# Kernel optimization log

Hardware: AMD Instinct MI355X
Metric: run time of the kernel (lower is better)

## Reference

```python
import jax, jax.numpy as jnp
import numpy as np

B, S, H, F, E, TOPK = 2, 2048, 1024, 512, 8, 2


def setup_inputs() -> dict:
    key = jax.random.key(0)
    k1, k2, k3, k4, k5 = jax.random.split(key, 5)
    s_h = 1.0 / np.sqrt(H)
    s_f = 1.0 / np.sqrt(F)
    return {
        "x": jax.random.normal(k1, (B, S, H), dtype=jnp.float32),
        "Wr": jax.random.normal(k2, (H, E), dtype=jnp.float32) * s_h,   # router
        "Wg": jax.random.normal(k3, (E, H, F), dtype=jnp.float32) * s_h,  # gate proj
        "Wu": jax.random.normal(k4, (E, H, F), dtype=jnp.float32) * s_h,  # up proj
        "Wd": jax.random.normal(k5, (E, F, H), dtype=jnp.float32) * s_f,  # down proj
        "topk": TOPK,
    }


def reference(x, Wr, Wg, Wu, Wd, topk):
    Bq, Sq, Hq = x.shape
    Eq = Wr.shape[1]
    xf = x.reshape(-1, Hq)                      # [T, H]
    logits = xf @ Wr                            # [T, E]
    probs = jax.nn.softmax(logits, axis=-1)
    w, idx = jax.lax.top_k(probs, topk)         # [T, topk]
    w = w / jnp.sum(w, axis=-1, keepdims=True)  # normalize top-k probs (Qwen3-style)
    # combine coefficients per (token, expert): scatter top-k weights
    coeff = jnp.sum(jax.nn.one_hot(idx, Eq, dtype=w.dtype) * w[..., None], axis=1)  # [T, E]
    # dense dispatch/combine (math-equivalent to per-expert gather + scatter-add)
    gate = jnp.einsum('th,ehf->tef', xf, Wg)    # [T, E, F]
    up = jnp.einsum('th,ehf->tef', xf, Wu)
    act = jax.nn.silu(gate) * up                # SwiGLU expert
    # apply combine weight before down-proj (linearity) to avoid a [T,E,H] temp
    out = jnp.einsum('tef,efh->th', act * coeff[:, :, None], Wd)
    return out.reshape(Bq, Sq, Hq)
```

## Files before the change

kernel.cpp:

```cpp
#include <hip/hip_runtime.h>
#include <hip/hip_bf16.h>

#define T_TOK    4096
#define H_DIM    1024
#define F_DIM    512
#define N_EXP    8
#define N_ASSIGN 8192
#define BM 128
#define BN 128
#define BK 64
#define MAX_TILES 80
#define GRID_MT   71

typedef __bf16 bf16x8 __attribute__((ext_vector_type(8)));
typedef __bf16 bf16x2 __attribute__((ext_vector_type(2)));
typedef float  f32x4  __attribute__((ext_vector_type(4)));

#define MFMA16(a, b, c) __builtin_amdgcn_mfma_f32_16x16x32_bf16((a), (b), (c), 0, 0, 0)

__device__ __forceinline__ void gl_lds16(const __bf16* g, __bf16* l) {
    __builtin_amdgcn_global_load_lds(
        (const __attribute__((address_space(1))) unsigned int*)g,
        (__attribute__((address_space(3))) unsigned int*)l,
        16, 0, 0);
}

__global__ __launch_bounds__(256) void routing_kernel(
    const float* __restrict__ x, const float* __restrict__ Wr,
    __bf16* __restrict__ xb, int* __restrict__ top_e, float* __restrict__ top_w)
{
    int wave = threadIdx.x >> 6, lane = threadIdx.x & 63;
    int t = blockIdx.x * 4 + wave;
    const float* xrow = x + (size_t)t * H_DIM;
    __bf16* xbrow = xb + (size_t)t * H_DIM;

    float part[N_EXP];
#pragma unroll
    for (int e = 0; e < N_EXP; ++e) part[e] = 0.f;

#pragma unroll
    for (int half = 0; half < 2; ++half) {
        int h0 = half * 512 + lane * 8;
        float4 v0 = *(const float4*)(xrow + h0);
        float4 v1 = *(const float4*)(xrow + h0 + 4);
        float xs[8] = {v0.x, v0.y, v0.z, v0.w, v1.x, v1.y, v1.z, v1.w};
        bf16x8 bv;
#pragma unroll
        for (int i = 0; i < 8; ++i) bv[i] = (__bf16)xs[i];
        *(bf16x8*)(xbrow + h0) = bv;
#pragma unroll
        for (int i = 0; i < 8; ++i) {
            const float4* wr = (const float4*)(Wr + (size_t)(h0 + i) * N_EXP);
            float4 w0 = wr[0], w1 = wr[1];
            part[0] += xs[i] * w0.x; part[1] += xs[i] * w0.y;
            part[2] += xs[i] * w0.z; part[3] += xs[i] * w0.w;
            part[4] += xs[i] * w1.x; part[5] += xs[i] * w1.y;
            part[6] += xs[i] * w1.z; part[7] += xs[i] * w1.w;
        }
    }
#pragma unroll
    for (int m = 1; m < 64; m <<= 1) {
#pragma unroll
        for (int e = 0; e < N_EXP; ++e) part[e] += __shfl_xor(part[e], m, 64);
    }
    if (lane == 0) {
        float v1 = -1e30f, v2 = -1e30f;
        int i1 = 0, i2 = 0;
#pragma unroll
        for (int e = 0; e < N_EXP; ++e) {
            float p = part[e];
            if (p > v1)      { v2 = v1; i2 = i1; v1 = p; i1 = e; }
            else if (p > v2) { v2 = p;  i2 = e; }
        }
        float w1 = 1.f / (1.f + __expf(v2 - v1));
        top_e[t * 2]     = i1;  top_e[t * 2 + 1] = i2;
        top_w[t * 2]     = w1;  top_w[t * 2 + 1] = 1.f - w1;
    }
}

__global__ __launch_bounds__(256) void scan_kernel(
    const int* __restrict__ top_e,
    int* __restrict__ tile_e, int* __restrict__ tile_m0, int* __restrict__ tile_cnt,
    int* __restrict__ n_tiles, int* __restrict__ tbase)
{
    __shared__ int hist[N_EXP][256];
    __shared__ int ebase[N_EXP];
    int tid = threadIdx.x;

    int c[N_EXP];
#pragma unroll
    for (int e = 0; e < N_EXP; ++e) c[e] = 0;
#pragma unroll 4
    for (int i = 0; i < 32; ++i) {
        int ee = top_e[tid * 32 + i];
#pragma unroll
        for (int e = 0; e < N_EXP; ++e) c[e] += (ee == e);
    }
#pragma unroll
    for (int e = 0; e < N_EXP; ++e) hist[e][tid] = c[e];
    __syncthreads();

    for (int s = 1; s < 256; s <<= 1) {
        int v[N_EXP];
#pragma unroll
        for (int e = 0; e < N_EXP; ++e) v[e] = (tid >= s) ? hist[e][tid - s] : 0;
        __syncthreads();
#pragma unroll
        for (int e = 0; e < N_EXP; ++e) hist[e][tid] += v[e];
        __syncthreads();
    }

    if (tid == 0) {
        int o = 0, nt = 0;
        for (int e = 0; e < N_EXP; ++e) {
            ebase[e] = o;
            int ne = hist[e][255];
            for (int m0 = 0; m0 < ne; m0 += BM) {
                tile_e[nt]   = e;
                tile_m0[nt]  = o + m0;
                tile_cnt[nt] = (ne - m0 < BM) ? (ne - m0) : BM;
                ++nt;
            }
            o += ne;
        }
        *n_tiles = nt;
    }
    __syncthreads();

#pragma unroll
    for (int e = 0; e < N_EXP; ++e)
        tbase[e * 256 + tid] = ebase[e] + hist[e][tid] - c[e];
}

__global__ __launch_bounds__(256) void scatter_kernel(
    const int* __restrict__ top_e, const float* __restrict__ top_w,
    const int* __restrict__ tbase,
    int* __restrict__ perm, float* __restrict__ wts, int* __restrict__ tokslot)
{
    int e = blockIdx.x, tid = threadIdx.x;
    int base = tbase[e * 256 + tid];
#pragma unroll 4
    for (int i = 0; i < 32; ++i) {
        int a = tid * 32 + i;
        if (top_e[a] == e) {
            perm[base]   = a >> 1;
            wts[base]    = top_w[a];
            tokslot[a]   = base;
            ++base;
        }
    }
}

__global__ __launch_bounds__(256) void transpose_kernel(
    const float* __restrict__ Wg, const float* __restrict__ Wu, const float* __restrict__ Wd,
    __bf16* __restrict__ Wcat, __bf16* __restrict__ Wdt)
{
    int z = blockIdx.z;
    const float* src; int R, C;
    if (z < 8)       { src = Wg + (size_t)z * H_DIM * F_DIM;        R = H_DIM; C = F_DIM; }
    else if (z < 16) { src = Wu + (size_t)(z - 8) * H_DIM * F_DIM;  R = H_DIM; C = F_DIM; }
    else             { src = Wd + (size_t)(z - 16) * F_DIM * H_DIM; R = F_DIM; C = H_DIM; }
    int c0 = blockIdx.x * 32, r0 = blockIdx.y * 64;
    if (c0 >= C || r0 >= R) return;
    __shared__ float tile[64][33];
    int tx = threadIdx.x & 31, ty = threadIdx.x >> 5;
#pragma unroll
    for (int i = 0; i < 8; ++i)
        tile[ty + 8 * i][tx] = src[(size_t)(r0 + ty + 8 * i) * C + c0 + tx];
    __syncthreads();
    if (z < 16) {
        int e = (z < 8) ? z : z - 8;
        int sel = (z < 8) ? 0 : 16;
        __bf16* dst = Wcat + (size_t)e * (2 * F_DIM) * H_DIM;
#pragma unroll
        for (int i = 0; i < 4; ++i) {
            int f = c0 + ty + 8 * i;
            int p = ((f >> 4) << 5) + (f & 15) + sel;
            bf16x2 v = { (__bf16)tile[2 * tx][ty + 8 * i], (__bf16)tile[2 * tx + 1][ty + 8 * i] };
            *(bf16x2*)&dst[(size_t)p * H_DIM + r0 + 2 * tx] = v;
        }
    } else {
        __bf16* dst = Wdt + (size_t)(z - 16) * H_DIM * F_DIM;
#pragma unroll
        for (int i = 0; i < 4; ++i) {
            bf16x2 v = { (__bf16)tile[2 * tx][ty + 8 * i], (__bf16)tile[2 * tx + 1][ty + 8 * i] };
            *(bf16x2*)&dst[(size_t)(c0 + ty + 8 * i) * F_DIM + r0 + 2 * tx] = v;
        }
    }
}

__global__ __launch_bounds__(256, 3) void gateup_kernel(
    const __bf16* __restrict__ xb, const __bf16* __restrict__ Wcat,
    const int* __restrict__ perm, const float* __restrict__ wts,
    const int* __restrict__ tile_e, const int* __restrict__ tile_m0, const int* __restrict__ tile_cnt,
    const int* __restrict__ n_tiles, __bf16* __restrict__ act)
{
    int mt = blockIdx.x >> 3;
    if (mt >= *n_tiles) return;
    int e = tile_e[mt], m0 = tile_m0[mt], mcnt = tile_cnt[mt];
    int n0 = (blockIdx.x & 7) * BN;

    __shared__ __align__(16) __bf16 As[BM * BK];
    __shared__ __align__(16) __bf16 Bs[BN * BK];
    __shared__ int   rowtok[BM];
    __shared__ float roww[BM];

    int tid = threadIdx.x;
    if (tid < BM) {
        int slot = m0 + ((tid < mcnt) ? tid : 0);
        rowtok[tid] = perm[slot];
        roww[tid]   = wts[slot];
    }
    __syncthreads();

    int wave = tid >> 6, lane = tid & 63;
    int srow   = wave * 8 + (lane >> 3);
    int schunk = (((lane & 7) ^ ((lane >> 3) & 7))) * 8;
    const __bf16* We = Wcat + (size_t)e * (2 * F_DIM) * H_DIM;
    const __bf16* aptr[4];
    const __bf16* bptr[4];
#pragma unroll
    for (int j = 0; j < 4; ++j) {
        int r = j * 32 + srow;
        aptr[j] = xb + (size_t)rowtok[r] * H_DIM + schunk;
        bptr[j] = We + (size_t)(n0 + r) * H_DIM + schunk;
    }
    __bf16* aLds = As + wave * 512;
    __bf16* bLds = Bs + wave * 512;

    int wm = wave & 1, wn = wave >> 1;
    int quad = lane >> 4, l16 = lane & 15;

    f32x4 acc[4][4];
#pragma unroll
    for (int a = 0; a < 4; ++a)
#pragma unroll
        for (int b = 0; b < 4; ++b) acc[a][b] = (f32x4){0.f, 0.f, 0.f, 0.f};

    for (int k0 = 0; k0 < H_DIM; k0 += BK) {
#pragma unroll
        for (int j = 0; j < 4; ++j) {
            gl_lds16(aptr[j] + k0, aLds + j * 2048);
            gl_lds16(bptr[j] + k0, bLds + j * 2048);
        }
        __syncthreads();
#pragma unroll
        for (int s = 0; s < 2; ++s) {
            int sw = (((quad + s * 4) ^ (l16 & 7))) * 8;
            bf16x8 af[4], bf[4];
#pragma unroll
            for (int im = 0; im < 4; ++im)
                af[im] = *(const bf16x8*)&As[(wm * 64 + im * 16 + l16) * 64 + sw];
#pragma unroll
            for (int in = 0; in < 4; ++in)
                bf[in] = *(const bf16x8*)&Bs[(wn * 64 + in * 16 + l16) * 64 + sw];
#pragma unroll
            for (int im = 0; im < 4; ++im)
#pragma unroll
                for (int in = 0; in < 4; ++in)
                    acc[im][in] = MFMA16(af[im], bf[in], acc[im][in]);
        }
        __syncthreads();
    }

    int fbase = (n0 >> 1) + wn * 32;
#pragma unroll
    for (int im = 0; im < 4; ++im) {
#pragma unroll
        for (int ip = 0; ip < 2; ++ip) {
            f32x4 g = acc[im][ip * 2], u = acc[im][ip * 2 + 1];
            int fcol = fbase + ip * 16 + l16;
#pragma unroll
            for (int r = 0; r < 4; ++r) {
                int rl = wm * 64 + im * 16 + quad * 4 + r;
                if (rl < mcnt) {
                    float gv = g[r], uv = u[r];
                    float sg = gv / (1.f + __expf(-gv));
                    act[(size_t)(m0 + rl) * F_DIM + fcol] = (__bf16)(sg * uv * roww[rl]);
                }
            }
        }
    }
}

__global__ __launch_bounds__(256, 3) void down_kernel(
    const __bf16* __restrict__ act, const __bf16* __restrict__ Wdt,
    const int* __restrict__ tile_e, const int* __restrict__ tile_m0, const int* __restrict__ tile_cnt,
    const int* __restrict__ n_tiles, float* __restrict__ P)
{
    int mt = blockIdx.x >> 3;
    if (mt >= *n_tiles) return;
    int e = tile_e[mt], m0 = tile_m0[mt], mcnt = tile_cnt[mt];
    int n0 = (blockIdx.x & 7) * BN;

    __shared__ __align__(16) __bf16 As[BM * BK];
    __shared__ __align__(16) __bf16 Bs[BN * BK];

    int tid = threadIdx.x;
    int wave = tid >> 6, lane = tid & 63;
    int srow   = wave * 8 + (lane >> 3);
    int schunk = (((lane & 7) ^ ((lane >> 3) & 7))) * 8;
    const __bf16* Wd_e = Wdt + (size_t)e * H_DIM * F_DIM;
    const __bf16* aptr[4];
    const __bf16* bptr[4];
#pragma unroll
    for (int j = 0; j < 4; ++j) {
        int r = j * 32 + srow;
        int ar = m0 + ((r < mcnt) ? r : 0);
        aptr[j] = act  + (size_t)ar * F_DIM + schunk;
        bptr[j] = Wd_e + (size_t)(n0 + r) * F_DIM + schunk;
    }
    __bf16* aLds = As + wave * 512;
    __bf16* bLds = Bs + wave * 512;

    int wm = wave & 1, wn = wave >> 1;
    int quad = lane >> 4, l16 = lane & 15;

    f32x4 acc[4][4];
#pragma unroll
    for (int a = 0; a < 4; ++a)
#pragma unroll
        for (int b = 0; b < 4; ++b) acc[a][b] = (f32x4){0.f, 0.f, 0.f, 0.f};

    for (int k0 = 0; k0 < F_DIM; k0 += BK) {
#pragma unroll
        for (int j = 0; j < 4; ++j) {
            gl_lds16(aptr[j] + k0, aLds + j * 2048);
            gl_lds16(bptr[j] + k0, bLds + j * 2048);
        }
        __syncthreads();
#pragma unroll
        for (int s = 0; s < 2; ++s) {
            int sw = (((quad + s * 4) ^ (l16 & 7))) * 8;
            bf16x8 af[4], bf[4];
#pragma unroll
            for (int im = 0; im < 4; ++im)
                af[im] = *(const bf16x8*)&As[(wm * 64 + im * 16 + l16) * 64 + sw];
#pragma unroll
            for (int in = 0; in < 4; ++in)
                bf[in] = *(const bf16x8*)&Bs[(wn * 64 + in * 16 + l16) * 64 + sw];
#pragma unroll
            for (int im = 0; im < 4; ++im)
#pragma unroll
                for (int in = 0; in < 4; ++in)
                    acc[im][in] = MFMA16(af[im], bf[in], acc[im][in]);
        }
        __syncthreads();
    }

#pragma unroll
    for (int im = 0; im < 4; ++im) {
#pragma unroll
        for (int in = 0; in < 4; ++in) {
            int col = n0 + wn * 64 + in * 16 + l16;
#pragma unroll
            for (int r = 0; r < 4; ++r) {
                int rl = wm * 64 + im * 16 + quad * 4 + r;
                if (rl < mcnt)
                    P[(size_t)(m0 + rl) * H_DIM + col] = acc[im][in][r];
            }
        }
    }
}

__global__ __launch_bounds__(256) void combine_kernel(
    const float* __restrict__ P, const int* __restrict__ tokslot,
    float* __restrict__ out)
{
    int wave = threadIdx.x >> 6, lane = threadIdx.x & 63;
    int t = blockIdx.x * 4 + wave;
    int s1 = tokslot[2 * t], s2 = tokslot[2 * t + 1];
    const f32x4* p1 = (const f32x4*)(P + (size_t)s1 * H_DIM);
    const f32x4* p2 = (const f32x4*)(P + (size_t)s2 * H_DIM);
    f32x4* o = (f32x4*)(out + (size_t)t * H_DIM);
#pragma unroll
    for (int i = 0; i < H_DIM / 4 / 64; ++i) {
        int idx = i * 64 + lane;
        f32x4 a = p1[idx], b = p2[idx];
        o[idx] = (f32x4){a.x + b.x, a.y + b.y, a.z + b.z, a.w + b.w};
    }
}

extern "C" void kernel_launch(void* const* d_in, const int* in_sizes, int n_in,
                              void* d_out, int out_size, void* d_ws, size_t ws_size,
                              hipStream_t stream)
{
    const float* x  = (const float*)d_in[0];
    const float* Wr = (const float*)d_in[1];
    const float* Wg = (const float*)d_in[2];
    const float* Wu = (const float*)d_in[3];
    const float* Wd = (const float*)d_in[4];
    float* out = (float*)d_out;

    char* ws = (char*)d_ws;
    size_t off = 0;
    auto carve = [&](size_t bytes) {
        char* p = ws + off;
        off = (off + bytes + 255) & ~(size_t)255;
        return p;
    };
    __bf16* xb   = (__bf16*)carve((size_t)T_TOK * H_DIM * 2);
    __bf16* Wcat = (__bf16*)carve((size_t)N_EXP * 2 * F_DIM * H_DIM * 2);
    __bf16* Wdt  = (__bf16*)carve((size_t)N_EXP * H_DIM * F_DIM * 2);
    __bf16* act  = (__bf16*)carve((size_t)N_ASSIGN * F_DIM * 2);
    float* P     = (float*)carve((size_t)N_ASSIGN * H_DIM * sizeof(float));
    int*   top_e = (int*)carve((size_t)T_TOK * 2 * sizeof(int));
    float* top_w = (float*)carve((size_t)T_TOK * 2 * sizeof(float));
    int*   perm  = (int*)carve((size_t)N_ASSIGN * sizeof(int));
    float* wts   = (float*)carve((size_t)N_ASSIGN * sizeof(float));
    int*  tokslot= (int*)carve((size_t)N_ASSIGN * sizeof(int));
    int*   tbase = (int*)carve((size_t)N_EXP * 256 * sizeof(int));
    int*   tl_e  = (int*)carve(MAX_TILES * sizeof(int));
    int*   tl_m0 = (int*)carve(MAX_TILES * sizeof(int));
    int*   tl_cn = (int*)carve(MAX_TILES * sizeof(int));
    int*   n_til = (int*)carve(sizeof(int));

    routing_kernel<<<T_TOK / 4, 256, 0, stream>>>(x, Wr, xb, top_e, top_w);
    scan_kernel<<<1, 256, 0, stream>>>(top_e, tl_e, tl_m0, tl_cn, n_til, tbase);
    scatter_kernel<<<N_EXP, 256, 0, stream>>>(top_e, top_w, tbase, perm, wts, tokslot);
    transpose_kernel<<<dim3(32, 16, 24), 256, 0, stream>>>(Wg, Wu, Wd, Wcat, Wdt);
    gateup_kernel<<<GRID_MT * 8, 256, 0, stream>>>(
        xb, Wcat, perm, wts, tl_e, tl_m0, tl_cn, n_til, act);
    down_kernel<<<GRID_MT * 8, 256, 0, stream>>>(
        act, Wdt, tl_e, tl_m0, tl_cn, n_til, P);
    combine_kernel<<<T_TOK / 4, 256, 0, stream>>>(P, tokslot, out);
}
```

Measured before the change: 206.1 us.

## Merge prep kernels, fuse scan with scatter, store down-proj partials in bf16

Folds the weight transpose and routing into one prep launch using a flat block index, and merges the scan and scatter kernels into a single per-expert kernel in which each block recomputes the histogram and scan. The down-projection partial outputs P are now written as bf16 instead of fp32, halving the bytes written by down_kernel and read by combine_kernel. This removes two launches and the tbase round-trip, at the cost of redundant scan work across eight blocks and extra rounding of the partials before the top-2 sum.

```diff
diff --git a/kernel.cpp b/kernel.cpp
--- a/kernel.cpp
+++ b/kernel.cpp
@@ -11,6 +11,7 @@
 #define BK 64
 #define MAX_TILES 80
 #define GRID_MT   71
+#define TR_BLOCKS (32 * 16 * 24)
 
 typedef __bf16 bf16x8 __attribute__((ext_vector_type(8)));
 typedef __bf16 bf16x2 __attribute__((ext_vector_type(2)));
@@ -25,12 +26,50 @@
         16, 0, 0);
 }
 
-__global__ __launch_bounds__(256) void routing_kernel(
-    const float* __restrict__ x, const float* __restrict__ Wr,
-    __bf16* __restrict__ xb, int* __restrict__ top_e, float* __restrict__ top_w)
-{
+__global__ __launch_bounds__(256) void prep_kernel(
+    const float* __restrict__ x,  const float* __restrict__ Wr,
+    const float* __restrict__ Wg, const float* __restrict__ Wu, const float* __restrict__ Wd,
+    __bf16* __restrict__ xb, int* __restrict__ top_e, float* __restrict__ top_w,
+    __bf16* __restrict__ Wcat, __bf16* __restrict__ Wdt)
+{
+    __shared__ float tile[64][33];
+    int b = blockIdx.x;
+    if (b < TR_BLOCKS) {
+        int z = b >> 9, rem = b & 511;
+        int c0 = (rem & 31) * 32, r0 = (rem >> 5) * 64;
+        const float* src; int R, C;
+        if (z < 8)       { src = Wg + (size_t)z * H_DIM * F_DIM;        R = H_DIM; C = F_DIM; }
+        else if (z < 16) { src = Wu + (size_t)(z - 8) * H_DIM * F_DIM;  R = H_DIM; C = F_DIM; }
+        else             { src = Wd + (size_t)(z - 16) * F_DIM * H_DIM; R = F_DIM; C = H_DIM; }
+        if (c0 >= C || r0 >= R) return;
+        int tx = threadIdx.x & 31, ty = threadIdx.x >> 5;
+#pragma unroll
+        for (int i = 0; i < 8; ++i)
+            tile[ty + 8 * i][tx] = src[(size_t)(r0 + ty + 8 * i) * C + c0 + tx];
+        __syncthreads();
+        if (z < 16) {
+            int e = (z < 8) ? z : z - 8;
+            int sel = (z < 8) ? 0 : 16;
+            __bf16* dst = Wcat + (size_t)e * (2 * F_DIM) * H_DIM;
+#pragma unroll
+            for (int i = 0; i < 4; ++i) {
+                int f = c0 + ty + 8 * i;
+                int p = ((f >> 4) << 5) + (f & 15) + sel;
+                bf16x2 v = { (__bf16)tile[2 * tx][ty + 8 * i], (__bf16)tile[2 * tx + 1][ty + 8 * i] };
+                *(bf16x2*)&dst[(size_t)p * H_DIM + r0 + 2 * tx] = v;
+            }
+        } else {
+            __bf16* dst = Wdt + (size_t)(z - 16) * H_DIM * F_DIM;
+#pragma unroll
+            for (int i = 0; i < 4; ++i) {
+                bf16x2 v = { (__bf16)tile[2 * tx][ty + 8 * i], (__bf16)tile[2 * tx + 1][ty + 8 * i] };
+                *(bf16x2*)&dst[(size_t)(c0 + ty + 8 * i) * F_DIM + r0 + 2 * tx] = v;
+            }
+        }
+        return;
+    }
     int wave = threadIdx.x >> 6, lane = threadIdx.x & 63;
-    int t = blockIdx.x * 4 + wave;
+    int t = (b - TR_BLOCKS) * 4 + wave;
     const float* xrow = x + (size_t)t * H_DIM;
     __bf16* xbrow = xb + (size_t)t * H_DIM;
 
@@ -78,14 +117,15 @@
     }
 }
 
-__global__ __launch_bounds__(256) void scan_kernel(
-    const int* __restrict__ top_e,
+__global__ __launch_bounds__(256) void sort_kernel(
+    const int* __restrict__ top_e, const float* __restrict__ top_w,
+    int* __restrict__ perm, float* __restrict__ wts, int* __restrict__ tokslot,
     int* __restrict__ tile_e, int* __restrict__ tile_m0, int* __restrict__ tile_cnt,
-    int* __restrict__ n_tiles, int* __restrict__ tbase)
+    int* __restrict__ n_tiles)
 {
     __shared__ int hist[N_EXP][256];
     __shared__ int ebase[N_EXP];
-    int tid = threadIdx.x;
+    int tid = threadIdx.x, myexp = blockIdx.x;
 
     int c[N_EXP];
 #pragma unroll
@@ -115,76 +155,29 @@
         for (int e = 0; e < N_EXP; ++e) {
             ebase[e] = o;
             int ne = hist[e][255];
-            for (int m0 = 0; m0 < ne; m0 += BM) {
-                tile_e[nt]   = e;
-                tile_m0[nt]  = o + m0;
-                tile_cnt[nt] = (ne - m0 < BM) ? (ne - m0) : BM;
-                ++nt;
+            if (myexp == 0) {
+                for (int m0 = 0; m0 < ne; m0 += BM) {
+                    tile_e[nt]   = e;
+                    tile_m0[nt]  = o + m0;
+                    tile_cnt[nt] = (ne - m0 < BM) ? (ne - m0) : BM;
+                    ++nt;
+                }
             }
             o += ne;
         }
-        *n_tiles = nt;
+        if (myexp == 0) *n_tiles = nt;
     }
     __syncthreads();
 
-#pragma unroll
-    for (int e = 0; e < N_EXP; ++e)
-        tbase[e * 256 + tid] = ebase[e] + hist[e][tid] - c[e];
-}
-
-__global__ __launch_bounds__(256) void scatter_kernel(
-    const int* __restrict__ top_e, const float* __restrict__ top_w,
-    const int* __restrict__ tbase,
-    int* __restrict__ perm, float* __restrict__ wts, int* __restrict__ tokslot)
-{
-    int e = blockIdx.x, tid = threadIdx.x;
-    int base = tbase[e * 256 + tid];
+    int base = ebase[myexp] + hist[myexp][tid] - c[myexp];
 #pragma unroll 4
     for (int i = 0; i < 32; ++i) {
         int a = tid * 32 + i;
-        if (top_e[a] == e) {
+        if (top_e[a] == myexp) {
             perm[base]   = a >> 1;
             wts[base]    = top_w[a];
             tokslot[a]   = base;
             ++base;
-        }
-    }
-}
-
-__global__ __launch_bounds__(256) void transpose_kernel(
-    const float* __restrict__ Wg, const float* __restrict__ Wu, const float* __restrict__ Wd,
-    __bf16* __restrict__ Wcat, __bf16* __restrict__ Wdt)
-{
-    int z = blockIdx.z;
-    const float* src; int R, C;
-    if (z < 8)       { src = Wg + (size_t)z * H_DIM * F_DIM;        R = H_DIM; C = F_DIM; }
-    else if (z < 16) { src = Wu + (size_t)(z - 8) * H_DIM * F_DIM;  R = H_DIM; C = F_DIM; }
-    else             { src = Wd + (size_t)(z - 16) * F_DIM * H_DIM; R = F_DIM; C = H_DIM; }
-    int c0 = blockIdx.x * 32, r0 = blockIdx.y * 64;
-    if (c0 >= C || r0 >= R) return;
-    __shared__ float tile[64][33];
-    int tx = threadIdx.x & 31, ty = threadIdx.x >> 5;
-#pragma unroll
-    for (int i = 0; i < 8; ++i)
-        tile[ty + 8 * i][tx] = src[(size_t)(r0 + ty + 8 * i) * C + c0 + tx];
-    __syncthreads();
-    if (z < 16) {
-        int e = (z < 8) ? z : z - 8;
-        int sel = (z < 8) ? 0 : 16;
-        __bf16* dst = Wcat + (size_t)e * (2 * F_DIM) * H_DIM;
-#pragma unroll
-        for (int i = 0; i < 4; ++i) {
-            int f = c0 + ty + 8 * i;
-            int p = ((f >> 4) << 5) + (f & 15) + sel;
-            bf16x2 v = { (__bf16)tile[2 * tx][ty + 8 * i], (__bf16)tile[2 * tx + 1][ty + 8 * i] };
-            *(bf16x2*)&dst[(size_t)p * H_DIM + r0 + 2 * tx] = v;
-        }
-    } else {
-        __bf16* dst = Wdt + (size_t)(z - 16) * H_DIM * F_DIM;
-#pragma unroll
-        for (int i = 0; i < 4; ++i) {
-            bf16x2 v = { (__bf16)tile[2 * tx][ty + 8 * i], (__bf16)tile[2 * tx + 1][ty + 8 * i] };
-            *(bf16x2*)&dst[(size_t)(c0 + ty + 8 * i) * F_DIM + r0 + 2 * tx] = v;
         }
     }
 }
@@ -286,7 +279,7 @@
 __global__ __launch_bounds__(256, 3) void down_kernel(
     const __bf16* __restrict__ act, const __bf16* __restrict__ Wdt,
     const int* __restrict__ tile_e, const int* __restrict__ tile_m0, const int* __restrict__ tile_cnt,
-    const int* __restrict__ n_tiles, float* __restrict__ P)
+    const int* __restrict__ n_tiles, __bf16* __restrict__ P)
 {
     int mt = blockIdx.x >> 3;
     if (mt >= *n_tiles) return;
@@ -357,27 +350,33 @@
             for (int r = 0; r < 4; ++r) {
                 int rl = wm * 64 + im * 16 + quad * 4 + r;
                 if (rl < mcnt)
-                    P[(size_t)(m0 + rl) * H_DIM + col] = acc[im][in][r];
+                    P[(size_t)(m0 + rl) * H_DIM + col] = (__bf16)acc[im][in][r];
             }
         }
     }
 }
 
 __global__ __launch_bounds__(256) void combine_kernel(
-    const float* __restrict__ P, const int* __restrict__ tokslot,
+    const __bf16* __restrict__ P, const int* __restrict__ tokslot,
     float* __restrict__ out)
 {
     int wave = threadIdx.x >> 6, lane = threadIdx.x & 63;
     int t = blockIdx.x * 4 + wave;
     int s1 = tokslot[2 * t], s2 = tokslot[2 * t + 1];
-    const f32x4* p1 = (const f32x4*)(P + (size_t)s1 * H_DIM);
-    const f32x4* p2 = (const f32x4*)(P + (size_t)s2 * H_DIM);
-    f32x4* o = (f32x4*)(out + (size_t)t * H_DIM);
-#pragma unroll
-    for (int i = 0; i < H_DIM / 4 / 64; ++i) {
+    const bf16x8* p1 = (const bf16x8*)(P + (size_t)s1 * H_DIM);
+    const bf16x8* p2 = (const bf16x8*)(P + (size_t)s2 * H_DIM);
+    float* o = out + (size_t)t * H_DIM;
+#pragma unroll
+    for (int i = 0; i < 2; ++i) {
         int idx = i * 64 + lane;
-        f32x4 a = p1[idx], b = p2[idx];
-        o[idx] = (f32x4){a.x + b.x, a.y + b.y, a.z + b.z, a.w + b.w};
+        bf16x8 a = p1[idx], b = p2[idx];
+        f32x4 lo, hi;
+#pragma unroll
+        for (int j = 0; j < 4; ++j) lo[j] = (float)a[j] + (float)b[j];
+#pragma unroll
+        for (int j = 0; j < 4; ++j) hi[j] = (float)a[4 + j] + (float)b[4 + j];
+        *(f32x4*)(o + idx * 8)     = lo;
+        *(f32x4*)(o + idx * 8 + 4) = hi;
     }
 }
 
@@ -403,22 +402,21 @@
     __bf16* Wcat = (__bf16*)carve((size_t)N_EXP * 2 * F_DIM * H_DIM * 2);
     __bf16* Wdt  = (__bf16*)carve((size_t)N_EXP * H_DIM * F_DIM * 2);
     __bf16* act  = (__bf16*)carve((size_t)N_ASSIGN * F_DIM * 2);
-    float* P     = (float*)carve((size_t)N_ASSIGN * H_DIM * sizeof(float));
+    __bf16* P    = (__bf16*)carve((size_t)N_ASSIGN * H_DIM * 2);
     int*   top_e = (int*)carve((size_t)T_TOK * 2 * sizeof(int));
     float* top_w = (float*)carve((size_t)T_TOK * 2 * sizeof(float));
     int*   perm  = (int*)carve((size_t)N_ASSIGN * sizeof(int));
     float* wts   = (float*)carve((size_t)N_ASSIGN * sizeof(float));
     int*  tokslot= (int*)carve((size_t)N_ASSIGN * sizeof(int));
-    int*   tbase = (int*)carve((size_t)N_EXP * 256 * sizeof(int));
     int*   tl_e  = (int*)carve(MAX_TILES * sizeof(int));
     int*   tl_m0 = (int*)carve(MAX_TILES * sizeof(int));
     int*   tl_cn = (int*)carve(MAX_TILES * sizeof(int));
     int*   n_til = (int*)carve(sizeof(int));
 
-    routing_kernel<<<T_TOK / 4, 256, 0, stream>>>(x, Wr, xb, top_e, top_w);
-    scan_kernel<<<1, 256, 0, stream>>>(top_e, tl_e, tl_m0, tl_cn, n_til, tbase);
-    scatter_kernel<<<N_EXP, 256, 0, stream>>>(top_e, top_w, tbase, perm, wts, tokslot);
-    transpose_kernel<<<dim3(32, 16, 24), 256, 0, stream>>>(Wg, Wu, Wd, Wcat, Wdt);
+    prep_kernel<<<TR_BLOCKS + T_TOK / 4, 256, 0, stream>>>(
+        x, Wr, Wg, Wu, Wd, xb, top_e, top_w, Wcat, Wdt);
+    sort_kernel<<<N_EXP, 256, 0, stream>>>(
+        top_e, top_w, perm, wts, tokslot, tl_e, tl_m0, tl_cn, n_til);
     gateup_kernel<<<GRID_MT * 8, 256, 0, stream>>>(
         xb, Wcat, perm, wts, tl_e, tl_m0, tl_cn, n_til, act);
     down_kernel<<<GRID_MT * 8, 256, 0, stream>>>(
```

Measured after the change: 206.7 us. Within noise of the previous version (+0.3%).
